# Kernel optimization log

Measured on AMD Instinct MI355X. Metric: run time of the kernel, lower is better.

Reference implementation:

```python
import jax, jax.numpy as jnp
import numpy as np

B, L, D, H = 2, 2048, 1024, 16
Dh = D // H


def setup_inputs() -> dict:
    key = jax.random.key(0)
    ks = jax.random.split(key, 9)
    s = 1.0 / np.sqrt(D)
    inp = {
        "x": jax.random.normal(ks[0], (B, L, D), dtype=jnp.float32),
        # True above the diagonal => masked (causal)
        "causal_mask": jnp.triu(jnp.ones((L, L), dtype=bool), k=1)[None, None],
        "wq": jax.random.uniform(ks[1], (D, D), jnp.float32, -s, s),
        "bq": jax.random.uniform(ks[2], (D,), jnp.float32, -s, s),
        "wk": jax.random.uniform(ks[3], (D, D), jnp.float32, -s, s),
        "bk": jax.random.uniform(ks[4], (D,), jnp.float32, -s, s),
        "wv": jax.random.uniform(ks[5], (D, D), jnp.float32, -s, s),
        "bv": jax.random.uniform(ks[6], (D,), jnp.float32, -s, s),
        "wo": jax.random.uniform(ks[7], (D, D), jnp.float32, -s, s),
        "bo": jax.random.uniform(ks[8], (D,), jnp.float32, -s, s),
    }
    return inp


def reference(x, causal_mask, wq, bq, wk, bk, wv, bv, wo, bo):
    # projections; weights stored [in, out]-style as [D, D] used as x @ W + b
    def proj(w, b):
        return (x @ w + b).reshape(B, L, H, Dh).transpose(0, 2, 1, 3)  # [B,H,L,Dh]

    q = proj(wq, bq)
    k = proj(wk, bk)
    v = proj(wv, bv)
    scale = jnp.sqrt(jnp.asarray(Dh, x.dtype))
    scores = jnp.einsum("bhqd,bhkd->bhqk", q, k) / scale  # [B,H,L,L]
    scores = jnp.where(causal_mask[:, :, :L, :L], -jnp.inf, scores)
    attn = jax.nn.softmax(scores, axis=-1)  # dropout p=0.0 (eval)
    out = jnp.einsum("bhqk,bhkd->bhqd", attn, v)
    out = out.transpose(0, 2, 1, 3).reshape(B, L, D)
    return out @ wo + bo
```

## Files before the change

### kernel.cpp

```cpp
#include <hip/hip_runtime.h>


typedef short v8s __attribute__((ext_vector_type(8)));
typedef __bf16 v8bf __attribute__((ext_vector_type(8)));
typedef float v4f __attribute__((ext_vector_type(4)));
typedef float v16f __attribute__((ext_vector_type(16)));
typedef unsigned int uint;

#define DEV static __device__ __forceinline__

DEV short f2bf(float f) {
  unsigned u = __builtin_bit_cast(unsigned, f);
  u += 0x7FFFu + ((u >> 16) & 1u);
  return (short)(u >> 16);
}

DEV uint pack2(float lo, float hi) {
  return (uint)(unsigned short)f2bf(lo) | ((uint)(unsigned short)f2bf(hi) << 16);
}

DEV v4f mfma16(v8s a, v8s b, v4f c) {
  return __builtin_amdgcn_mfma_f32_16x16x32_bf16(
      __builtin_bit_cast(v8bf, a), __builtin_bit_cast(v8bf, b), c, 0, 0, 0);
}

DEV v16f mfma32(v8s a, v8s b, v16f c) {
  return __builtin_amdgcn_mfma_f32_32x32x16_bf16(
      __builtin_bit_cast(v8bf, a), __builtin_bit_cast(v8bf, b), c, 0, 0, 0);
}

#define GLDS16(g, l)                                                         \
  __builtin_amdgcn_global_load_lds(                                          \
      (__attribute__((address_space(1))) void*)(g),                          \
      (__attribute__((address_space(3))) void*)(l), 16, 0, 0)

__global__ __launch_bounds__(256) void k_cvt(const float* __restrict__ x,
                                             short* __restrict__ xb) {
  int i = blockIdx.x * 256 + threadIdx.x;
  float4 v = reinterpret_cast<const float4*>(x)[i];
  short4 o;
  o.x = f2bf(v.x); o.y = f2bf(v.y); o.z = f2bf(v.z); o.w = f2bf(v.w);
  reinterpret_cast<short4*>(xb)[i] = o;
}

__global__ __launch_bounds__(256) void k_tw(const float* __restrict__ wq,
                                            const float* __restrict__ wk,
                                            const float* __restrict__ wv,
                                            const float* __restrict__ wo,
                                            short* __restrict__ wqkvT,
                                            short* __restrict__ woT) {
  __shared__ float t[32][33];
  int wi = blockIdx.z;
  const float* src = (wi == 0) ? wq : (wi == 1) ? wk : (wi == 2) ? wv : wo;
  short* dst = (wi < 3) ? (wqkvT + wi * 1024 * 1024) : woT;
  int n0 = blockIdx.x * 32, k0 = blockIdx.y * 32;
  int tx = threadIdx.x, ty = threadIdx.y;
#pragma unroll
  for (int i = 0; i < 4; i++)
    t[ty + i * 8][tx] = src[(k0 + ty + i * 8) * 1024 + n0 + tx];
  __syncthreads();
#pragma unroll
  for (int i = 0; i < 4; i++)
    dst[(n0 + ty + i * 8) * 1024 + k0 + tx] = f2bf(t[tx][ty + i * 8]);
}

template <int MODE>
__global__ __launch_bounds__(256) void k_gemm(
    const short* __restrict__ A, const short* __restrict__ BT,
    const float* __restrict__ b0, const float* __restrict__ b1,
    const float* __restrict__ b2, short* __restrict__ Qo,
    short* __restrict__ Ko, short* __restrict__ VTo,
    float* __restrict__ outF) {
  constexpr int K = 1024;
  __shared__ short As[128 * 64], Bs[128 * 64];
  __shared__ short SL[64 * 132];
  const int tid = threadIdx.x;
  const int w = tid >> 6, lane = tid & 63;
  const int wr = w >> 1, wc = w & 1;
  const int bm = blockIdx.y, bn = blockIdx.x;
  const int lr = lane & 15, lg = lane >> 4;

  const int rA = tid >> 3;
  const int cbs = ((tid & 7) * 16) ^ ((rA & 7) << 4);
  const short* pA[4];
  const short* pB[4];
#pragma unroll
  for (int i = 0; i < 4; i++) {
    pA[i] = A + (size_t)(bm * 128 + rA + i * 32) * K + (cbs >> 1);
    pB[i] = BT + (size_t)(bn * 128 + rA + i * 32) * K + (cbs >> 1);
  }

  v4f acc[4][4] = {};
  for (int kt = 0; kt < K / 64; ++kt) {
#pragma unroll
    for (int i = 0; i < 4; i++) {
      GLDS16(pA[i] + kt * 64, As + i * 2048 + w * 512);
      GLDS16(pB[i] + kt * 64, Bs + i * 2048 + w * 512);
    }
    __syncthreads();
#pragma unroll
    for (int ks = 0; ks < 2; ++ks) {
      v8s af[4], bf[4];
#pragma unroll
      for (int mf = 0; mf < 4; mf++) {
        int R = wr * 64 + mf * 16 + lr;
        int byo = (R * 128 + ks * 64 + lg * 16) ^ ((R & 7) << 4);
        af[mf] = *reinterpret_cast<const v8s*>(
            reinterpret_cast<const char*>(As) + byo);
      }
#pragma unroll
      for (int nf = 0; nf < 4; nf++) {
        int R = wc * 64 + nf * 16 + lr;
        int byo = (R * 128 + ks * 64 + lg * 16) ^ ((R & 7) << 4);
        bf[nf] = *reinterpret_cast<const v8s*>(
            reinterpret_cast<const char*>(Bs) + byo);
      }
      __builtin_amdgcn_s_setprio(1);
#pragma unroll
      for (int mf = 0; mf < 4; mf++)
#pragma unroll
        for (int nf = 0; nf < 4; nf++)
          acc[mf][nf] = mfma16(af[mf], bf[nf], acc[mf][nf]);
      __builtin_amdgcn_s_setprio(0);
    }
    __syncthreads();
  }

  if constexpr (MODE == 0) {
    if (bn < 16) {
#pragma unroll
      for (int mf = 0; mf < 4; mf++) {
#pragma unroll
        for (int nf = 0; nf < 4; nf++) {
#pragma unroll
          for (int r = 0; r < 4; r++) {
            int mrow = bm * 128 + wr * 64 + mf * 16 + lg * 4 + r;
            int ncol = bn * 128 + wc * 64 + nf * 16 + lr;
            int which = ncol >> 10, d = ncol & 1023;
            float v = acc[mf][nf][r] + ((which == 0) ? b0[d] : b1[d]);
            int h = d >> 6, dh = d & 63;
            int bb = mrow >> 11, lp = mrow & 2047;
            if (which == 0)
              Qo[((size_t)(bb * 16 + h) * 2048 + lp) * 64 + dh] =
                  f2bf(v * 0.18033688011112043f);
            else
              Ko[((size_t)(bb * 16 + h) * 2048 + lp) * 64 + dh] = f2bf(v);
          }
        }
      }
    } else {
      const int bb = bm >> 4;
      const int lp0 = (bm & 15) * 128;
#pragma unroll
      for (int hh = 0; hh < 2; ++hh) {
        if (wc == hh) {
#pragma unroll
          for (int mf = 0; mf < 4; mf++)
#pragma unroll
            for (int nf = 0; nf < 4; nf++)
#pragma unroll
              for (int r = 0; r < 4; r++) {
                int mrow_l = wr * 64 + mf * 16 + lg * 4 + r;
                int ncol_l = nf * 16 + lr;
                int d = (bn - 16) * 128 + hh * 64 + ncol_l;
                SL[ncol_l * 132 + mrow_l] = f2bf(acc[mf][nf][r] + b2[d]);
              }
        }
        __syncthreads();
        int h = (bn - 16) * 2 + hh;
        int row = tid >> 2;
#pragma unroll
        for (int q = 0; q < 4; q++) {
          int col = ((tid & 3) + q * 4) * 8;
          *reinterpret_cast<v8s*>(
              VTo + ((size_t)(bb * 16 + h) * 64 + row) * 2048 + lp0 + col) =
              *reinterpret_cast<const v8s*>(SL + row * 132 + col);
        }
        __syncthreads();
      }
    }
  } else {
#pragma unroll
    for (int mf = 0; mf < 4; mf++)
#pragma unroll
      for (int nf = 0; nf < 4; nf++)
#pragma unroll
        for (int r = 0; r < 4; r++) {
          int mrow = bm * 128 + wr * 64 + mf * 16 + lg * 4 + r;
          int ncol = bn * 128 + wc * 64 + nf * 16 + lr;
          outF[(size_t)mrow * 1024 + ncol] = acc[mf][nf][r] + b0[ncol];
        }
  }
}

__global__ __launch_bounds__(256) void k_flash(const short* __restrict__ Qg,
                                               const short* __restrict__ Kg,
                                               const short* __restrict__ VTg,
                                               short* __restrict__ ctx) {
  __shared__ short Kl[2][128 * 64];
  __shared__ short Vl[2][64 * 128];
  const int tid = threadIdx.x, w = tid >> 6, lane = tid & 63;
  const int l31 = lane & 31, hi = lane >> 5;
  const int bh = blockIdx.x;
  const int y = blockIdx.y;
  const int qt = (y < 8) ? y : 23 - y;
  const int q = qt * 128 + w * 32 + l31;

  v8s qf[4];
  {
    const short* qrow = Qg + ((size_t)bh * 2048 + q) * 64 + hi * 8;
#pragma unroll
    for (int dc = 0; dc < 4; dc++)
      qf[dc] = *reinterpret_cast<const v8s*>(qrow + dc * 16);
  }

  float m = -1e30f, l = 0.f;
  v16f o0 = {}, o1 = {};

  const short* kb = Kg + (size_t)bh * 2048 * 64;
  const short* vb = VTg + (size_t)bh * 64 * 2048;

  const int lKr = lane >> 3;
  const int lKc = ((lane & 7) ^ lKr) * 8;
  const int lVr = lane >> 4;
  const int w4 = w * 4;

  const int nt = qt + 1;
  int c = 0;
#define STAGE(kt_, cc_)                                                        \
  {                                                                            \
    _Pragma("unroll") for (int i = 0; i < 4; i++) {                            \
      int ii = w4 + i;                                                         \
      GLDS16(kb + (size_t)((kt_)*128 + ii * 8 + lKr) * 64 + lKc,               \
             &Kl[cc_][ii * 512]);                                              \
      int vr = ii * 4 + lVr;                                                   \
      GLDS16(vb + (size_t)vr * 2048 + (kt_)*128 + ((lane & 15) ^ (vr & 7)) * 8,\
             &Vl[cc_][ii * 512]);                                              \
    }                                                                          \
  }
  STAGE(0, 0);

  const int rx = (l31 & 7) << 4;
  const int krb = l31 * 128;
  const int vrb = l31 * 256;

  for (int kt = 0; kt < nt; ++kt) {
    __syncthreads();
    if (kt + 1 < nt) STAGE(kt + 1, c ^ 1);

    v16f s0 = {}, s1 = {}, s2 = {}, s3 = {};
    const char* Klc = reinterpret_cast<const char*>(Kl[c]);
    __builtin_amdgcn_s_setprio(1);
#pragma unroll
    for (int dc = 0; dc < 4; dc++) {
      int cb = (dc * 32 + hi * 16) ^ rx;
      v8s k0 = *reinterpret_cast<const v8s*>(Klc + krb + cb);
      v8s k1 = *reinterpret_cast<const v8s*>(Klc + 4096 + krb + cb);
      v8s k2 = *reinterpret_cast<const v8s*>(Klc + 8192 + krb + cb);
      v8s k3 = *reinterpret_cast<const v8s*>(Klc + 12288 + krb + cb);
      s0 = mfma32(k0, qf[dc], s0);
      s1 = mfma32(k1, qf[dc], s1);
      s2 = mfma32(k2, qf[dc], s2);
      s3 = mfma32(k3, qf[dc], s3);
    }
    __builtin_amdgcn_s_setprio(0);

    if (kt == qt) {
      int kb0 = kt * 128 + 4 * hi;
#pragma unroll
      for (int r = 0; r < 16; r++) {
        int kv = kb0 + (r & 3) + 8 * (r >> 2);
        if (kv > q) s0[r] = -1e30f;
        if (kv + 32 > q) s1[r] = -1e30f;
        if (kv + 64 > q) s2[r] = -1e30f;
        if (kv + 96 > q) s3[r] = -1e30f;
      }
    }

    float pm = s0[0];
#pragma unroll
    for (int r = 1; r < 16; r++) pm = fmaxf(pm, s0[r]);
#pragma unroll
    for (int r = 0; r < 16; r++) pm = fmaxf(pm, s1[r]);
#pragma unroll
    for (int r = 0; r < 16; r++) pm = fmaxf(pm, s2[r]);
#pragma unroll
    for (int r = 0; r < 16; r++) pm = fmaxf(pm, s3[r]);
    pm = fmaxf(pm, __shfl_xor(pm, 32, 64));
    if (__any(pm - m > 8.0f)) {
      float mn = fmaxf(m, pm);
      float alpha = __builtin_amdgcn_exp2f(m - mn);
      m = mn;
      l *= alpha;
#pragma unroll
      for (int r = 0; r < 16; r++) { o0[r] *= alpha; o1[r] *= alpha; }
    }
    float rs = 0.f;
#pragma unroll
    for (int r = 0; r < 16; r++) {
      s0[r] = __builtin_amdgcn_exp2f(s0[r] - m); rs += s0[r];
    }
#pragma unroll
    for (int r = 0; r < 16; r++) {
      s1[r] = __builtin_amdgcn_exp2f(s1[r] - m); rs += s1[r];
    }
#pragma unroll
    for (int r = 0; r < 16; r++) {
      s2[r] = __builtin_amdgcn_exp2f(s2[r] - m); rs += s2[r];
    }
#pragma unroll
    for (int r = 0; r < 16; r++) {
      s3[r] = __builtin_amdgcn_exp2f(s3[r] - m); rs += s3[r];
    }
    l += rs + __shfl_xor(rs, 32, 64);

    uint W0[8], W1[8], W2[8], W3[8];
#pragma unroll
    for (int t = 0; t < 8; t++) {
      W0[t] = pack2(s0[2 * t], s0[2 * t + 1]);
      W1[t] = pack2(s1[2 * t], s1[2 * t + 1]);
      W2[t] = pack2(s2[2 * t], s2[2 * t + 1]);
      W3[t] = pack2(s3[2 * t], s3[2 * t + 1]);
    }

    const char* Vlc = reinterpret_cast<const char*>(Vl[c]);
    __builtin_amdgcn_s_setprio(1);
#pragma unroll
    for (int kc = 0; kc < 8; kc++) {
      const uint* Wp = (kc < 2) ? W0 : (kc < 4) ? W1 : (kc < 6) ? W2 : W3;
      int base = (kc & 1) * 4;
      uint S0 = Wp[base + 0], S1 = Wp[base + 1];
      uint S2 = Wp[base + 2], S3 = Wp[base + 3];
      uint x0 = __shfl_xor(hi ? S0 : S2, 32, 64);
      uint x1 = __shfl_xor(hi ? S1 : S3, 32, 64);
      uint4 uf;
      uf.x = hi ? x0 : S0;
      uf.y = hi ? x1 : S1;
      uf.z = hi ? S2 : x0;
      uf.w = hi ? S3 : x1;
      v8s pf = __builtin_bit_cast(v8s, uf);
      int cb = (kc * 32 + hi * 16) ^ rx;
      v8s v0 = *reinterpret_cast<const v8s*>(Vlc + vrb + cb);
      v8s v1 = *reinterpret_cast<const v8s*>(Vlc + 8192 + vrb + cb);
      o0 = mfma32(v0, pf, o0);
      o1 = mfma32(v1, pf, o1);
    }
    __builtin_amdgcn_s_setprio(0);
    c ^= 1;
  }

  const int h = bh & 15, bb = bh >> 4;
  float inv = 1.0f / l;
  short* orow = ctx + ((size_t)(bb * 2048 + q)) * 1024 + h * 64;
#pragma unroll
  for (int df = 0; df < 2; df++) {
#pragma unroll
    for (int g = 0; g < 4; g++) {
      short4 st;
      const v16f& o = df ? o1 : o0;
      st.x = f2bf(o[g * 4 + 0] * inv);
      st.y = f2bf(o[g * 4 + 1] * inv);
      st.z = f2bf(o[g * 4 + 2] * inv);
      st.w = f2bf(o[g * 4 + 3] * inv);
      *reinterpret_cast<short4*>(orow + df * 32 + 8 * g + 4 * hi) = st;
    }
  }
}

extern "C" void kernel_launch(void* const* d_in, const int* in_sizes, int n_in,
                              void* d_out, int out_size, void* d_ws,
                              size_t ws_size, hipStream_t stream) {
  (void)in_sizes; (void)n_in; (void)out_size; (void)ws_size;
  const float* x = (const float*)d_in[0];
  const float* wq = (const float*)d_in[2];
  const float* bq = (const float*)d_in[3];
  const float* wk = (const float*)d_in[4];
  const float* bk = (const float*)d_in[5];
  const float* wv = (const float*)d_in[6];
  const float* bv = (const float*)d_in[7];
  const float* wo = (const float*)d_in[8];
  const float* bo = (const float*)d_in[9];

  char* ws = (char*)d_ws;
  short* xb = (short*)(ws);
  short* wqkvT = (short*)(ws + (8u << 20));
  short* woT = (short*)(ws + (14u << 20));
  short* Qb = (short*)(ws + (16u << 20));
  short* Kb = (short*)(ws + (24u << 20));
  short* VTb = (short*)(ws + (32u << 20));
  short* ctx = xb;
  float* out = (float*)d_out;

  k_cvt<<<4096, 256, 0, stream>>>(x, xb);
  k_tw<<<dim3(32, 32, 4), dim3(32, 8), 0, stream>>>(wq, wk, wv, wo, wqkvT, woT);
  k_gemm<0><<<dim3(24, 32), 256, 0, stream>>>(xb, wqkvT, bq, bk, bv, Qb, Kb,
                                              VTb, nullptr);
  k_flash<<<dim3(32, 16), 256, 0, stream>>>(Qb, Kb, VTb, ctx);
  k_gemm<1><<<dim3(8, 32), 256, 0, stream>>>(ctx, woT, bo, nullptr, nullptr,
                                             nullptr, nullptr, nullptr, out);
}
```

Baseline: 212.7 us.

## Merge prep kernels, alias GEMM LDS, swizzle GEMM blocks, tree-reduce softmax

Folds the input conversion and weight transpose into one launch, which removes a kernel launch. The GEMM epilogue staging buffer now aliases the A tile, cutting LDS use so more blocks can be resident. The GEMM uses a 1D grid with a block-index remap that groups row tiles for L2 reuse. In the flash kernel, the row max and row sum become tree reductions to shorten dependency chains. Aliasing SL onto As needs a barrier before reuse, and it is not visible whether the hidden code has one.

```diff
diff --git a/kernel.cpp b/kernel.cpp
--- a/kernel.cpp
+++ b/kernel.cpp
@@ -34,34 +34,35 @@
       (__attribute__((address_space(1))) void*)(g),                          \
       (__attribute__((address_space(3))) void*)(l), 16, 0, 0)
 
-__global__ __launch_bounds__(256) void k_cvt(const float* __restrict__ x,
-                                             short* __restrict__ xb) {
-  int i = blockIdx.x * 256 + threadIdx.x;
-  float4 v = reinterpret_cast<const float4*>(x)[i];
-  short4 o;
-  o.x = f2bf(v.x); o.y = f2bf(v.y); o.z = f2bf(v.z); o.w = f2bf(v.w);
-  reinterpret_cast<short4*>(xb)[i] = o;
-}
-
-__global__ __launch_bounds__(256) void k_tw(const float* __restrict__ wq,
-                                            const float* __restrict__ wk,
-                                            const float* __restrict__ wv,
-                                            const float* __restrict__ wo,
-                                            short* __restrict__ wqkvT,
-                                            short* __restrict__ woT) {
-  __shared__ float t[32][33];
-  int wi = blockIdx.z;
-  const float* src = (wi == 0) ? wq : (wi == 1) ? wk : (wi == 2) ? wv : wo;
-  short* dst = (wi < 3) ? (wqkvT + wi * 1024 * 1024) : woT;
-  int n0 = blockIdx.x * 32, k0 = blockIdx.y * 32;
-  int tx = threadIdx.x, ty = threadIdx.y;
-#pragma unroll
-  for (int i = 0; i < 4; i++)
-    t[ty + i * 8][tx] = src[(k0 + ty + i * 8) * 1024 + n0 + tx];
-  __syncthreads();
-#pragma unroll
-  for (int i = 0; i < 4; i++)
-    dst[(n0 + ty + i * 8) * 1024 + k0 + tx] = f2bf(t[tx][ty + i * 8]);
+__global__ __launch_bounds__(256) void k_prep(
+    const float* __restrict__ x, short* __restrict__ xb,
+    const float* __restrict__ wq, const float* __restrict__ wk,
+    const float* __restrict__ wv, const float* __restrict__ wo,
+    short* __restrict__ wqkvT, short* __restrict__ woT) {
+  const int bid = blockIdx.x, tid = threadIdx.x;
+  if (bid < 4096) {
+    int i = bid * 256 + tid;
+    float4 v = reinterpret_cast<const float4*>(x)[i];
+    short4 o;
+    o.x = f2bf(v.x); o.y = f2bf(v.y); o.z = f2bf(v.z); o.w = f2bf(v.w);
+    reinterpret_cast<short4*>(xb)[i] = o;
+  } else {
+    __shared__ float t[32][33];
+    int b2 = bid - 4096;
+    int wi = b2 >> 10;
+    int rem = b2 & 1023;
+    const float* src = (wi == 0) ? wq : (wi == 1) ? wk : (wi == 2) ? wv : wo;
+    short* dst = (wi < 3) ? (wqkvT + wi * 1024 * 1024) : woT;
+    int n0 = (rem & 31) * 32, k0 = (rem >> 5) * 32;
+    int tx = tid & 31, ty = tid >> 5;
+#pragma unroll
+    for (int i = 0; i < 4; i++)
+      t[ty + i * 8][tx] = src[(k0 + ty + i * 8) * 1024 + n0 + tx];
+    __syncthreads();
+#pragma unroll
+    for (int i = 0; i < 4; i++)
+      dst[(n0 + ty + i * 8) * 1024 + k0 + tx] = f2bf(t[tx][ty + i * 8]);
+  }
 }
 
 template <int MODE>
@@ -72,12 +73,17 @@
     short* __restrict__ Ko, short* __restrict__ VTo,
     float* __restrict__ outF) {
   constexpr int K = 1024;
-  __shared__ short As[128 * 64], Bs[128 * 64];
-  __shared__ short SL[64 * 132];
+  __shared__ short AB[2][128 * 64];
+  short* As = AB[0];
+  short* Bs = AB[1];
+  short* SL = AB[0];
   const int tid = threadIdx.x;
   const int w = tid >> 6, lane = tid & 63;
   const int wr = w >> 1, wc = w & 1;
-  const int bm = blockIdx.y, bn = blockIdx.x;
+  const int id = blockIdx.x;
+  const int pos = id >> 3;
+  const int bm = (id & 7) * 4 + (pos & 3);
+  const int bn = pos >> 2;
   const int lr = lane & 15, lg = lane >> 4;
 
   const int rA = tid >> 3;
@@ -277,15 +283,16 @@
       }
     }
 
-    float pm = s0[0];
-#pragma unroll
-    for (int r = 1; r < 16; r++) pm = fmaxf(pm, s0[r]);
-#pragma unroll
-    for (int r = 0; r < 16; r++) pm = fmaxf(pm, s1[r]);
-#pragma unroll
-    for (int r = 0; r < 16; r++) pm = fmaxf(pm, s2[r]);
-#pragma unroll
-    for (int r = 0; r < 16; r++) pm = fmaxf(pm, s3[r]);
+    float a[16];
+#pragma unroll
+    for (int r = 0; r < 16; r++)
+      a[r] = fmaxf(fmaxf(s0[r], s1[r]), fmaxf(s2[r], s3[r]));
+#pragma unroll
+    for (int off = 8; off > 0; off >>= 1)
+#pragma unroll
+      for (int r = 0; r < 8; r++)
+        if (r < off) a[r] = fmaxf(a[r], a[r + off]);
+    float pm = a[0];
     pm = fmaxf(pm, __shfl_xor(pm, 32, 64));
     if (__any(pm - m > 8.0f)) {
       float mn = fmaxf(m, pm);
@@ -295,23 +302,23 @@
 #pragma unroll
       for (int r = 0; r < 16; r++) { o0[r] *= alpha; o1[r] *= alpha; }
     }
-    float rs = 0.f;
 #pragma unroll
     for (int r = 0; r < 16; r++) {
-      s0[r] = __builtin_amdgcn_exp2f(s0[r] - m); rs += s0[r];
-    }
-#pragma unroll
-    for (int r = 0; r < 16; r++) {
-      s1[r] = __builtin_amdgcn_exp2f(s1[r] - m); rs += s1[r];
-    }
-#pragma unroll
-    for (int r = 0; r < 16; r++) {
-      s2[r] = __builtin_amdgcn_exp2f(s2[r] - m); rs += s2[r];
-    }
-#pragma unroll
-    for (int r = 0; r < 16; r++) {
-      s3[r] = __builtin_amdgcn_exp2f(s3[r] - m); rs += s3[r];
-    }
+      s0[r] = __builtin_amdgcn_exp2f(s0[r] - m);
+      s1[r] = __builtin_amdgcn_exp2f(s1[r] - m);
+      s2[r] = __builtin_amdgcn_exp2f(s2[r] - m);
+      s3[r] = __builtin_amdgcn_exp2f(s3[r] - m);
+    }
+    float b[16];
+#pragma unroll
+    for (int r = 0; r < 16; r++)
+      b[r] = (s0[r] + s1[r]) + (s2[r] + s3[r]);
+#pragma unroll
+    for (int off = 8; off > 0; off >>= 1)
+#pragma unroll
+      for (int r = 0; r < 8; r++)
+        if (r < off) b[r] = b[r] + b[r + off];
+    float rs = b[0];
     l += rs + __shfl_xor(rs, 32, 64);
 
     uint W0[8], W1[8], W2[8], W3[8];
@@ -391,11 +398,10 @@
   short* ctx = xb;
   float* out = (float*)d_out;
 
-  k_cvt<<<4096, 256, 0, stream>>>(x, xb);
-  k_tw<<<dim3(32, 32, 4), dim3(32, 8), 0, stream>>>(wq, wk, wv, wo, wqkvT, woT);
-  k_gemm<0><<<dim3(24, 32), 256, 0, stream>>>(xb, wqkvT, bq, bk, bv, Qb, Kb,
-                                              VTb, nullptr);
+  k_prep<<<8192, 256, 0, stream>>>(x, xb, wq, wk, wv, wo, wqkvT, woT);
+  k_gemm<0><<<768, 256, 0, stream>>>(xb, wqkvT, bq, bk, bv, Qb, Kb,
+                                     VTb, nullptr);
   k_flash<<<dim3(32, 16), 256, 0, stream>>>(Qb, Kb, VTb, ctx);
-  k_gemm<1><<<dim3(8, 32), 256, 0, stream>>>(ctx, woT, bo, nullptr, nullptr,
-                                             nullptr, nullptr, nullptr, out);
-}
+  k_gemm<1><<<256, 256, 0, stream>>>(ctx, woT, bo, nullptr, nullptr,
+                                     nullptr, nullptr, nullptr, out);
+}
```

Result: no change. 215.7 us (+1.4%).
